# Performance work log

Measured on AMD Instinct MI355X. Metric: run time of the kernel, lower is better.

The kernel has to match this reference:

```python
import jax, jax.numpy as jnp
import numpy as np
from jax import lax

DIM = 512
ATT_DIM = 512
N_HEADS = 8
HEAD_DIM = ATT_DIM // N_HEADS
SEQ = 4096


def q_rsqrt(x):
    # quake-style fast inverse sqrt with one Newton iteration (matches torch module)
    y = np.asarray((x,), dtype=np.float32)
    x2 = y * 0.5
    i = y.view(np.int32)
    i = np.right_shift(i, 1)
    i = 1597463007 - i
    y = i.view(np.float32)
    y = y * (1.5 - x2 * y * y)
    return float(y[0])

SCALING = q_rsqrt(HEAD_DIM)  # fast-approx 1/sqrt(head_dim)

# Schraudolph fast-exp constants (pulp-trainlib fastexp_gist)
GIST_A = 12102203.17133801  # 2^23 / ln(2)
GIST_B = 1064986823.0       # bias with correction term
GIST_C = 8388608.0          # underflow cutoff -> 0
GIST_D = 2139095040.0       # overflow clamp (float32 inf bits)


def fastexp_gist(x):
    t = GIST_A * x + GIST_B
    t = jnp.where(t < GIST_C, 0.0, jnp.where(t > GIST_D, GIST_D, t))
    return lax.bitcast_convert_type(t.astype(jnp.int32), jnp.float32)


def softmax_fastexp(s):
    m = jnp.max(s, axis=-1, keepdims=True)
    e = fastexp_gist(s - m)
    return e / jnp.sum(e, axis=-1, keepdims=True)


def setup_inputs() -> dict:
    key = jax.random.key(0)
    ks = jax.random.split(key, 8)
    std = 0.02
    return {
        "x": jax.random.normal(ks[0], (SEQ, DIM), dtype=jnp.float32),
        "Wq": jax.random.normal(ks[1], (ATT_DIM, DIM), dtype=jnp.float32) * std,
        "bq": jnp.zeros((ATT_DIM,), dtype=jnp.float32),
        "Wk": jax.random.normal(ks[2], (ATT_DIM, DIM), dtype=jnp.float32) * std,
        "bk": jnp.zeros((ATT_DIM,), dtype=jnp.float32),
        "Wv": jax.random.normal(ks[3], (ATT_DIM, DIM), dtype=jnp.float32) * std,
        "bv": jnp.zeros((ATT_DIM,), dtype=jnp.float32),
        "Wout": jax.random.normal(ks[4], (DIM, ATT_DIM), dtype=jnp.float32) * std,
        "tgt_len": SEQ,
    }


def reference(x, Wq, bq, Wk, bk, Wv, bv, Wout, tgt_len):
    # projections (torch Linear: y = x @ W.T + b)
    q = (x @ Wq.T + bq).reshape(tgt_len, N_HEADS, HEAD_DIM).transpose(1, 0, 2)  # [H,L,d]
    k = (x @ Wk.T + bk).reshape(tgt_len, N_HEADS, HEAD_DIM).transpose(1, 0, 2)
    v = (x @ Wv.T + bv).reshape(tgt_len, N_HEADS, HEAD_DIM).transpose(1, 0, 2)
    scores = jnp.einsum('hld,hmd->hlm', q, k) * SCALING  # [H,L,L]
    probs = softmax_fastexp(scores)
    out = jnp.einsum('hlm,hmd->hld', probs, v)           # [H,L,d]
    out = out.transpose(1, 0, 2).reshape(tgt_len, ATT_DIM)
    return out @ Wout.T  # proj_out has no bias
```

## Files before the change

### kernel.cpp

```cpp
#include <hip/hip_runtime.h>
#include <hip/hip_bf16.h>
#include <string.h>

#define SEQ 4096
#define DIM 512
#define NH  8
#define HD  64
#define SEQP (SEQ + 128)
#define NT  (SEQ/64)
#define KSPLIT 4
#define KCHUNK (SEQ/KSPLIT)
#define KTILES (KCHUNK/64)
#define PMSPLIT 8
#define KCHUNK_A (SEQ/PMSPLIT)
#define KTILES_A (KCHUNK_A/64)

typedef __attribute__((ext_vector_type(4))) float  f32x4;
typedef __attribute__((ext_vector_type(8))) short  bf16x8;
typedef __attribute__((ext_vector_type(4))) short  s16x4;
typedef __attribute__((ext_vector_type(2))) unsigned int u32x2;

__device__ __forceinline__ unsigned short f2bfh(float f){
    union { __hip_bfloat16 h; unsigned short u; } cv;
    cv.h = __float2bfloat16(f);
    return cv.u;
}

__device__ __forceinline__ bf16x8 cvt8(f32x4 lo, f32x4 hi){
    bf16x8 r;
    r[0]=(short)f2bfh(lo[0]); r[1]=(short)f2bfh(lo[1]);
    r[2]=(short)f2bfh(lo[2]); r[3]=(short)f2bfh(lo[3]);
    r[4]=(short)f2bfh(hi[0]); r[5]=(short)f2bfh(hi[1]);
    r[6]=(short)f2bfh(hi[2]); r[7]=(short)f2bfh(hi[3]);
    return r;
}

__device__ __forceinline__ bf16x8 load8f(const float* p){
    f32x4 lo = *(const f32x4*)p;
    f32x4 hi = *(const f32x4*)(p+4);
    return cvt8(lo, hi);
}

#define FENCE_LDS() asm volatile("s_waitcnt lgkmcnt(0)" ::: "memory")

__global__ __launch_bounds__(256) void cvt5_kernel(
    const float* __restrict__ x,  const float* __restrict__ wq,
    const float* __restrict__ wk, const float* __restrict__ wv,
    const float* __restrict__ wo,
    unsigned short* __restrict__ xb,  unsigned short* __restrict__ wqb,
    unsigned short* __restrict__ wkb, unsigned short* __restrict__ wvb,
    unsigned short* __restrict__ wob)
{
    int b = blockIdx.x;
    const float* src; unsigned short* dst; int base;
    if (b < 1024){ src = x; dst = xb; base = b; }
    else {
        int t  = (b - 1024) >> 7;
        base   = (b - 1024) & 127;
        src = (t==0) ? wq  : (t==1) ? wk  : (t==2) ? wv  : wo;
        dst = (t==0) ? wqb : (t==1) ? wkb : (t==2) ? wvb : wob;
    }
    size_t i = ((size_t)base*256 + threadIdx.x)*8;
    f32x4 lo = *(const f32x4*)(src + i);
    f32x4 hi = *(const f32x4*)(src + i + 4);
    *(bf16x8*)(dst + i) = cvt8(lo, hi);
}

__global__ __launch_bounds__(256, 4) void proj_qkv_b_kernel(
    const unsigned short* __restrict__ xb,
    const unsigned short* __restrict__ Wqb, const float* __restrict__ bq,
    const unsigned short* __restrict__ Wkb, const float* __restrict__ bk,
    const unsigned short* __restrict__ Wvb, const float* __restrict__ bv,
    unsigned short* __restrict__ Qb, unsigned short* __restrict__ Kh,
    unsigned short* __restrict__ Vtp)
{
    __shared__ __align__(16) unsigned short xs[128*64];
    __shared__ __align__(16) unsigned short wsh[64*64];

    const int z = blockIdx.z;
    const unsigned short* W = (z==0) ? Wqb : ((z==1) ? Wkb : Wvb);
    const float* bb = (z==0) ? bq : ((z==1) ? bk : bv);
    const int tid = threadIdx.x;
    const int wv  = tid >> 6;
    const int l   = tid & 63;
    const int g   = l >> 4;
    const int l15 = l & 15;
    const int l7  = l15 & 7;
    const int r0b = blockIdx.x * 128;
    const int c0  = blockIdx.y * 64;
    const int hy  = blockIdx.y;

    const int sc  = tid & 7;
    const int sr  = tid >> 3;
    const int scs = (sc ^ (sr & 7)) * 8;

    f32x4 acc[2][4];
    #pragma unroll
    for(int s=0;s<2;s++)
        #pragma unroll
        for(int d=0;d<4;d++) acc[s][d] = (f32x4){0.f,0.f,0.f,0.f};

    bf16x8 xf[4], wf[2];
    #pragma unroll
    for(int j=0;j<4;j++)
        xf[j] = *(const bf16x8*)(xb + (size_t)(r0b + sr + 32*j)*DIM + sc*8);
    #pragma unroll
    for(int j=0;j<2;j++)
        wf[j] = *(const bf16x8*)(W + (size_t)(c0 + sr + 32*j)*DIM + sc*8);

    for(int t=0;t<8;t++){
        #pragma unroll
        for(int j=0;j<4;j++)
            *(bf16x8*)&xs[(sr + 32*j)*64 + scs] = xf[j];
        #pragma unroll
        for(int j=0;j<2;j++)
            *(bf16x8*)&wsh[(sr + 32*j)*64 + scs] = wf[j];
        __syncthreads();
        if(t+1 < 8){
            const int kt = (t+1)*64;
            #pragma unroll
            for(int j=0;j<4;j++)
                xf[j] = *(const bf16x8*)(xb + (size_t)(r0b + sr + 32*j)*DIM + kt + sc*8);
            #pragma unroll
            for(int j=0;j<2;j++)
                wf[j] = *(const bf16x8*)(W + (size_t)(c0 + sr + 32*j)*DIM + kt + sc*8);
        }
        #pragma unroll
        for(int kh=0;kh<2;kh++){
            bf16x8 a[2];
            #pragma unroll
            for(int s=0;s<2;s++){
                const int row = wv*32 + s*16 + l15;
                a[s] = *(const bf16x8*)&xs[row*64 + (((kh*4+g) ^ l7)*8)];
            }
            #pragma unroll
            for(int d=0;d<4;d++){
                const int row = d*16 + l15;
                bf16x8 b = *(const bf16x8*)&wsh[row*64 + (((kh*4+g) ^ l7)*8)];
                #pragma unroll
                for(int s=0;s<2;s++)
                    acc[s][d] = __builtin_amdgcn_mfma_f32_16x16x32_bf16(a[s], b, acc[s][d], 0,0,0);
            }
        }
        __syncthreads();
    }

    const int r0 = r0b + wv*32;
    #pragma unroll
    for(int d=0;d<4;d++){
        float bias = bb[c0 + d*16 + l15];
        #pragma unroll
        for(int s=0;s<2;s++){
            if(z == 2){
                s16x4 pk;
                #pragma unroll
                for(int r=0;r<4;r++) pk[r] = (short)f2bfh(acc[s][d][r] + bias);
                *(s16x4*)(Vtp + ((size_t)hy*HD + d*16+l15)*SEQP + r0 + s*16 + g*4) = pk;
            } else if(z == 1){
                #pragma unroll
                for(int r=0;r<4;r++)
                    Kh[((size_t)hy*SEQ + r0+s*16+g*4+r)*HD + d*16 + l15] =
                        f2bfh(acc[s][d][r] + bias);
            } else {
                #pragma unroll
                for(int r=0;r<4;r++)
                    Qb[(size_t)(r0+s*16+g*4+r)*DIM + c0 + d*16 + l15] =
                        f2bfh(acc[s][d][r] + bias);
            }
        }
    }
}

__global__ __launch_bounds__(256) void proj_qkv_kernel(
    const float* __restrict__ x,
    const float* __restrict__ Wq, const float* __restrict__ bq,
    const float* __restrict__ Wk, const float* __restrict__ bk,
    const float* __restrict__ Wv, const float* __restrict__ bv,
    unsigned short* __restrict__ Qb, unsigned short* __restrict__ Kh,
    unsigned short* __restrict__ Vtp)
{
    const int z = blockIdx.z;
    const float* W  = (z==0) ? Wq : ((z==1) ? Wk : Wv);
    const float* bb = (z==0) ? bq : ((z==1) ? bk : bv);
    const int wv  = threadIdx.x >> 6;
    const int l   = threadIdx.x & 63;
    const int g   = l >> 4;
    const int l15 = l & 15;
    const int r0  = blockIdx.x * 128 + wv * 32;
    const int c0  = blockIdx.y * 64;
    const int hy  = blockIdx.y;

    f32x4 acc[2][4];
    #pragma unroll
    for(int s=0;s<2;s++)
        #pragma unroll
        for(int d=0;d<4;d++) acc[s][d] = (f32x4){0.f,0.f,0.f,0.f};

    for(int kt=0; kt<DIM; kt+=32){
        bf16x8 a[2];
        #pragma unroll
        for(int s=0;s<2;s++)
            a[s] = load8f(x + (size_t)(r0+s*16+l15)*DIM + kt + g*8);
        #pragma unroll
        for(int d=0;d<4;d++){
            bf16x8 b = load8f(W + (size_t)(c0+d*16+l15)*DIM + kt + g*8);
            #pragma unroll
            for(int s=0;s<2;s++)
                acc[s][d] = __builtin_amdgcn_mfma_f32_16x16x32_bf16(a[s], b, acc[s][d], 0,0,0);
        }
    }

    #pragma unroll
    for(int d=0;d<4;d++){
        float bias = bb[c0 + d*16 + l15];
        #pragma unroll
        for(int s=0;s<2;s++){
            if(z == 2){
                s16x4 pk;
                #pragma unroll
                for(int r=0;r<4;r++) pk[r] = (short)f2bfh(acc[s][d][r] + bias);
                *(s16x4*)(Vtp + ((size_t)hy*HD + d*16+l15)*SEQP + r0 + s*16 + g*4) = pk;
            } else if(z == 1){
                #pragma unroll
                for(int r=0;r<4;r++)
                    Kh[((size_t)hy*SEQ + r0+s*16+g*4+r)*HD + d*16 + l15] =
                        f2bfh(acc[s][d][r] + bias);
            } else {
                #pragma unroll
                for(int r=0;r<4;r++)
                    Qb[(size_t)(r0+s*16+g*4+r)*DIM + c0 + d*16 + l15] =
                        f2bfh(acc[s][d][r] + bias);
            }
        }
    }
}

__global__ __launch_bounds__(512, 4) void attn_max_kernel(
    const unsigned short* __restrict__ Qb,
    const unsigned short* __restrict__ Kh,
    float* __restrict__ Pm)
{
    __shared__ __align__(16) unsigned short kb[2][64*64];

    const int tid = threadIdx.x;
    const int wv  = tid >> 6;
    const int l   = tid & 63;
    const int g   = l >> 4;
    const int l15 = l & 15;
    const int l7  = l15 & 7;
    const int h   = blockIdx.x & 7;
    const int kz  = (blockIdx.x >> 3) & 7;
    const int Rw  = (blockIdx.x >> 6) * 256 + wv * 32;
    const int kbase = kz * KCHUNK_A;

    const unsigned short* Khh = Kh + (size_t)h*SEQ*HD;
    const int sr  = tid >> 3, sc = tid & 7;
    const int scs = (sc ^ (sr & 7)) * 8;
    const int lA  = sr*64 + scs;

    bf16x8 aq[2][2];
    #pragma unroll
    for(int s=0;s<2;s++)
        #pragma unroll
        for(int kh=0;kh<2;kh++)
            aq[s][kh] = *(const bf16x8*)(Qb + (size_t)(Rw+s*16+l15)*DIM + h*HD + kh*32 + g*8);

    float mx[2];
    mx[0] = mx[1] = -3.0e38f;

    bf16x8 krA = *(const bf16x8*)(Khh + (size_t)(kbase+sr)*HD + sc*8);
    *(bf16x8*)&kb[0][lA] = krA;
    __syncthreads();

    for(int t=0;t<KTILES_A;t++){
        const int cur = t & 1;
        if(t+1 < KTILES_A)
            krA = *(const bf16x8*)(Khh + (size_t)(kbase+(t+1)*64+sr)*HD + sc*8);
        #pragma unroll
        for(int ks=0;ks<4;ks++){
            const int krow = ks*16 + l15;
            bf16x8 b0 = *(const bf16x8*)&kb[cur][krow*64 + ((g     ^ l7)*8)];
            bf16x8 b1 = *(const bf16x8*)&kb[cur][krow*64 + (((4+g) ^ l7)*8)];
            #pragma unroll
            for(int s=0;s<2;s++){
                f32x4 acc = (f32x4){0.f,0.f,0.f,0.f};
                acc = __builtin_amdgcn_mfma_f32_16x16x32_bf16(b0, aq[s][0], acc, 0,0,0);
                acc = __builtin_amdgcn_mfma_f32_16x16x32_bf16(b1, aq[s][1], acc, 0,0,0);
                #pragma unroll
                for(int r=0;r<4;r++) mx[s] = fmaxf(mx[s], acc[r]);
            }
        }
        if(t+1 < KTILES_A)
            *(bf16x8*)&kb[cur^1][lA] = krA;
        __syncthreads();
    }
    #pragma unroll
    for(int s=0;s<2;s++){
        mx[s] = fmaxf(mx[s], __shfl_xor(mx[s], 16, 64));
        mx[s] = fmaxf(mx[s], __shfl_xor(mx[s], 32, 64));
    }

    if(l < 16){
        Pm[(size_t)(h*PMSPLIT + kz)*SEQ + Rw + l15]      = mx[0];
        Pm[(size_t)(h*PMSPLIT + kz)*SEQ + Rw + 16 + l15] = mx[1];
    }
}

#define PSTRIDE 68

__global__ __launch_bounds__(512, 4) void attn_pv_kernel(
    const unsigned short* __restrict__ Qb,
    const unsigned short* __restrict__ Kh,
    const unsigned short* __restrict__ Vtp,
    const float* __restrict__ Pm,
    float* __restrict__ numf,
    float* __restrict__ denf,
    float k1f)
{
    __shared__ __align__(16) unsigned short kb[2][64*64];
    __shared__ __align__(16) unsigned short vb[2][64*64];
    __shared__ __align__(16) unsigned short pb[8][32*PSTRIDE];

    const int tid = threadIdx.x;
    const int wv  = tid >> 6;
    const int l   = tid & 63;
    const int g   = l >> 4;
    const int l15 = l & 15;
    const int l7  = l15 & 7;
    const int h   = blockIdx.x & 7;
    const int kz  = (blockIdx.x >> 3) & 3;
    const int Rw  = (blockIdx.x >> 5) * 256 + wv * 32;
    const int kbase = kz * KCHUNK;

    const unsigned short* Khh = Kh  + (size_t)h*SEQ*HD;
    const unsigned short* Vh  = Vtp + (size_t)h*HD*SEQP;

    const int sr  = tid >> 3, sc = tid & 7;
    const int scs = (sc ^ (sr & 7)) * 8;
    const int lA  = sr*64 + scs;

    bf16x8 aq[2][2];
    #pragma unroll
    for(int s=0;s<2;s++)
        #pragma unroll
        for(int kh=0;kh<2;kh++)
            aq[s][kh] = *(const bf16x8*)(Qb + (size_t)(Rw+s*16+l15)*DIM + h*HD + kh*32 + g*8);

    float crow[2];
    #pragma unroll
    for(int s=0;s<2;s++){
        const int row = Rw + s*16 + l15;
        float m = Pm[(size_t)(h*PMSPLIT+0)*SEQ + row];
        #pragma unroll
        for(int p=1;p<PMSPLIT;p++)
            m = fmaxf(m, Pm[(size_t)(h*PMSPLIT+p)*SEQ + row]);
        crow[s] = 1064986823.0f - k1f*m;
    }

    f32x4 oacc[2][4];
    #pragma unroll
    for(int s=0;s<2;s++)
        #pragma unroll
        for(int d=0;d<4;d++) oacc[s][d] = (f32x4){0.f,0.f,0.f,0.f};
    f32x4 dacc[2];
    dacc[0] = (f32x4){0.f,0.f,0.f,0.f};
    dacc[1] = (f32x4){0.f,0.f,0.f,0.f};

    bf16x8 ones;
    #pragma unroll
    for(int j=0;j<8;j++) ones[j] = (short)0x3F80;

    bf16x8 krA = *(const bf16x8*)(Khh + (size_t)(kbase+sr)*HD + sc*8);
    bf16x8 vrA = *(const bf16x8*)(Vh  + (size_t)sr*SEQP + kbase + sc*8);
    *(bf16x8*)&kb[0][lA] = krA;
    *(bf16x8*)&vb[0][lA] = vrA;
    __syncthreads();

    for(int t=0;t<KTILES;t++){
        const int cur = t & 1;
        if(t+1 < KTILES){
            const int k0n = kbase + (t+1)*64;
            krA = *(const bf16x8*)(Khh + (size_t)(k0n+sr)*HD + sc*8);
            vrA = *(const bf16x8*)(Vh  + (size_t)sr*SEQP + k0n + sc*8);
        }
        #pragma unroll
        for(int ks=0;ks<4;ks++){
            const int krow = ks*16 + l15;
            bf16x8 b0 = *(const bf16x8*)&kb[cur][krow*64 + ((g     ^ l7)*8)];
            bf16x8 b1 = *(const bf16x8*)&kb[cur][krow*64 + (((4+g) ^ l7)*8)];
            #pragma unroll
            for(int s=0;s<2;s++){
                f32x4 acc = (f32x4){0.f,0.f,0.f,0.f};
                acc = __builtin_amdgcn_mfma_f32_16x16x32_bf16(b0, aq[s][0], acc, 0,0,0);
                acc = __builtin_amdgcn_mfma_f32_16x16x32_bf16(b1, aq[s][1], acc, 0,0,0);
                unsigned int w0, w1;
                {
                    float t0 = fmaf(k1f, acc[0], crow[s]);
                    float t1 = fmaf(k1f, acc[1], crow[s]);
                    float t2 = fmaf(k1f, acc[2], crow[s]);
                    float t3 = fmaf(k1f, acc[3], crow[s]);
                    unsigned int p0 = f2bfh(__int_as_float((int)t0));
                    unsigned int p1 = f2bfh(__int_as_float((int)t1));
                    unsigned int p2 = f2bfh(__int_as_float((int)t2));
                    unsigned int p3 = f2bfh(__int_as_float((int)t3));
                    w0 = p0 | (p1 << 16);
                    w1 = p2 | (p3 << 16);
                }
                u32x2 pw; pw[0] = w0; pw[1] = w1;
                *(u32x2*)&pb[wv][(s*16+l15)*PSTRIDE + ks*16 + g*4] = pw;
            }
        }
        FENCE_LDS();

        __builtin_amdgcn_s_setprio(1);
        #pragma unroll
        for(int ks2=0; ks2<2; ks2++){
            bf16x8 pa[2];
            #pragma unroll
            for(int s=0;s<2;s++)
                pa[s] = *(const bf16x8*)&pb[wv][(s*16+l15)*PSTRIDE + ks2*32 + g*8];
            #pragma unroll
            for(int s=0;s<2;s++)
                dacc[s] = __builtin_amdgcn_mfma_f32_16x16x32_bf16(pa[s], ones, dacc[s], 0,0,0);
            #pragma unroll
            for(int d=0;d<4;d++){
                const int vrow = d*16 + l15;
                bf16x8 bv_ = *(const bf16x8*)&vb[cur][vrow*64 + (((ks2*4+g) ^ l7)*8)];
                #pragma unroll
                for(int s=0;s<2;s++)
                    oacc[s][d] = __builtin_amdgcn_mfma_f32_16x16x32_bf16(pa[s], bv_, oacc[s][d], 0,0,0);
            }
        }
        __builtin_amdgcn_s_setprio(0);

        if(t+1 < KTILES){
            *(bf16x8*)&kb[cur^1][lA] = krA;
            *(bf16x8*)&vb[cur^1][lA] = vrA;
        }
        __syncthreads();
    }

    #pragma unroll
    for(int s=0;s<2;s++)
        #pragma unroll
        for(int d=0;d<4;d++)
            #pragma unroll
            for(int r=0;r<4;r++)
                numf[(size_t)kz*SEQ*DIM + (size_t)(Rw+s*16+g*4+r)*DIM + h*HD + d*16 + l15]
                    = oacc[s][d][r];
    if(l15 == 0){
        #pragma unroll
        for(int s=0;s<2;s++)
            #pragma unroll
            for(int r=0;r<4;r++)
                denf[(size_t)kz*SEQ*NH + (size_t)(Rw+s*16+g*4+r)*NH + h] = dacc[s][r];
    }
}

__global__ __launch_bounds__(256) void attn_merge_kernel(
    const float* __restrict__ numf,
    const float* __restrict__ denf,
    unsigned short* __restrict__ Ab)
{
    const size_t NS = (size_t)SEQ*DIM;
    int idx = blockIdx.x*256 + threadIdx.x;
    int row = idx >> 7;
    int dg  = (idx & 127) << 2;
    int h   = dg >> 6;

    float d0 = denf[(size_t)0*SEQ*NH + (size_t)row*NH + h];
    float d1 = denf[(size_t)1*SEQ*NH + (size_t)row*NH + h];
    float d2 = denf[(size_t)2*SEQ*NH + (size_t)row*NH + h];
    float d3 = denf[(size_t)3*SEQ*NH + (size_t)row*NH + h];
    float inv = 1.0f / (((d0 + d1) + d2) + d3);

    f32x4 n0 = *(const f32x4*)(numf + 0*NS + (size_t)row*DIM + dg);
    f32x4 n1 = *(const f32x4*)(numf + 1*NS + (size_t)row*DIM + dg);
    f32x4 n2 = *(const f32x4*)(numf + 2*NS + (size_t)row*DIM + dg);
    f32x4 n3 = *(const f32x4*)(numf + 3*NS + (size_t)row*DIM + dg);
    f32x4 s = ((n0 + n1) + n2) + n3;

    s16x4 o;
    #pragma unroll
    for(int j=0;j<4;j++) o[j] = (short)f2bfh(s[j] * inv);
    *(s16x4*)(Ab + (size_t)row*DIM + dg) = o;
}

__global__ __launch_bounds__(256, 2) void attn_kernel(
    const unsigned short* __restrict__ Qb,
    const unsigned short* __restrict__ Kh,
    const unsigned short* __restrict__ Vtp,
    unsigned short* __restrict__ Ab,
    float k1f)
{
    __shared__ __align__(16) unsigned short kbf[2][64*64];
    __shared__ __align__(16) unsigned short vbf[2][64*64];
    __shared__ __align__(16) unsigned short pbf[4][16*68];

    const int tid = threadIdx.x;
    const int wv  = tid >> 6;
    const int l   = tid & 63;
    const int g   = l >> 4;
    const int l15 = l & 15;
    const int l7  = l15 & 7;
    const int h   = blockIdx.x & 7;
    const int Rw  = (blockIdx.x >> 3) * 64 + wv * 16;

    const unsigned short* Khh = Kh  + (size_t)h*SEQ*HD;
    const unsigned short* Vh  = Vtp + (size_t)h*HD*SEQP;

    const int sr  = tid >> 3;
    const int sc  = tid & 7;
    const int scs = (sc ^ (sr & 7)) * 8;
    const int ldsA = sr*64 + scs;
    const int ldsB = (sr+32)*64 + scs;

    bf16x8 aq[2];
    #pragma unroll
    for(int kh=0;kh<2;kh++)
        aq[kh] = *(const bf16x8*)(Qb + (size_t)(Rw+l15)*DIM + h*HD + kh*32 + g*8);

    bf16x8 krA, krB, vrA, vrB;

    float mx[4];
    mx[0]=mx[1]=mx[2]=mx[3]=-3.0e38f;

    krA = *(const bf16x8*)(Khh + (size_t)sr*HD      + sc*8);
    krB = *(const bf16x8*)(Khh + (size_t)(sr+32)*HD + sc*8);
    *(bf16x8*)&kbf[0][ldsA] = krA;
    *(bf16x8*)&kbf[0][ldsB] = krB;
    __syncthreads();

    for(int t=0;t<NT;t++){
        const int cur = t & 1;
        if(t+1 < NT){
            const unsigned short* kp = Khh + (size_t)((t+1)*64)*HD;
            krA = *(const bf16x8*)(kp + (size_t)sr*HD      + sc*8);
            krB = *(const bf16x8*)(kp + (size_t)(sr+32)*HD + sc*8);
        }
        #pragma unroll
        for(int ks=0;ks<4;ks++){
            const int krow = ks*16 + l15;
            bf16x8 b0 = *(const bf16x8*)&kbf[cur][krow*64 + ((g     ^ l7)*8)];
            bf16x8 b1 = *(const bf16x8*)&kbf[cur][krow*64 + (((4+g) ^ l7)*8)];
            f32x4 acc = (f32x4){0.f,0.f,0.f,0.f};
            acc = __builtin_amdgcn_mfma_f32_16x16x32_bf16(aq[0], b0, acc, 0,0,0);
            acc = __builtin_amdgcn_mfma_f32_16x16x32_bf16(aq[1], b1, acc, 0,0,0);
            #pragma unroll
            for(int r=0;r<4;r++) mx[r] = fmaxf(mx[r], acc[r]);
        }
        if(t+1 < NT){
            *(bf16x8*)&kbf[cur^1][ldsA] = krA;
            *(bf16x8*)&kbf[cur^1][ldsB] = krB;
        }
        __syncthreads();
    }
    #pragma unroll
    for(int off=1; off<16; off<<=1)
        #pragma unroll
        for(int r=0;r<4;r++)
            mx[r] = fmaxf(mx[r], __shfl_xor(mx[r], off, 64));
    float crow[4];
    #pragma unroll
    for(int r=0;r<4;r++) crow[r] = 1064986823.0f - k1f*mx[r];

    f32x4 oacc[4];
    #pragma unroll
    for(int d=0;d<4;d++) oacc[d] = (f32x4){0.f,0.f,0.f,0.f};
    f32x4 dacc = (f32x4){0.f,0.f,0.f,0.f};

    bf16x8 ones;
    #pragma unroll
    for(int j=0;j<8;j++) ones[j] = (short)0x3F80;

    krA = *(const bf16x8*)(Khh + (size_t)sr*HD        + sc*8);
    krB = *(const bf16x8*)(Khh + (size_t)(sr+32)*HD   + sc*8);
    vrA = *(const bf16x8*)(Vh  + (size_t)sr*SEQP      + sc*8);
    vrB = *(const bf16x8*)(Vh  + (size_t)(sr+32)*SEQP + sc*8);
    *(bf16x8*)&kbf[0][ldsA] = krA;  *(bf16x8*)&kbf[0][ldsB] = krB;
    *(bf16x8*)&vbf[0][ldsA] = vrA;  *(bf16x8*)&vbf[0][ldsB] = vrB;
    __syncthreads();

    for(int t=0;t<NT;t++){
        const int cur = t & 1;
        if(t+1 < NT){
            const int k0n = (t+1)*64;
            krA = *(const bf16x8*)(Khh + (size_t)(k0n + sr)*HD    + sc*8);
            krB = *(const bf16x8*)(Khh + (size_t)(k0n + sr+32)*HD + sc*8);
            vrA = *(const bf16x8*)(Vh  + (size_t)sr*SEQP      + k0n + sc*8);
            vrB = *(const bf16x8*)(Vh  + (size_t)(sr+32)*SEQP + k0n + sc*8);
        }
        #pragma unroll
        for(int ks=0;ks<4;ks++){
            const int krow = ks*16 + l15;
            bf16x8 b0 = *(const bf16x8*)&kbf[cur][krow*64 + ((g     ^ l7)*8)];
            bf16x8 b1 = *(const bf16x8*)&kbf[cur][krow*64 + (((4+g) ^ l7)*8)];
            f32x4 acc = (f32x4){0.f,0.f,0.f,0.f};
            acc = __builtin_amdgcn_mfma_f32_16x16x32_bf16(aq[0], b0, acc, 0,0,0);
            acc = __builtin_amdgcn_mfma_f32_16x16x32_bf16(aq[1], b1, acc, 0,0,0);
            #pragma unroll
            for(int r=0;r<4;r++){
                float tt = fmaf(k1f, acc[r], crow[r]);
                pbf[wv][(g*4+r)*68 + ks*16 + l15] = f2bfh(__int_as_float((int)tt));
            }
        }
        FENCE_LDS();

        #pragma unroll
        for(int ks2=0; ks2<2; ks2++){
            bf16x8 pa = *(const bf16x8*)&pbf[wv][l15*68 + ks2*32 + g*8];
            dacc = __builtin_amdgcn_mfma_f32_16x16x32_bf16(pa, ones, dacc, 0,0,0);
            #pragma unroll
            for(int d=0;d<4;d++){
                const int vrow = d*16 + l15;
                bf16x8 bv_ = *(const bf16x8*)&vbf[cur][vrow*64 + (((ks2*4+g) ^ l7)*8)];
                oacc[d] = __builtin_amdgcn_mfma_f32_16x16x32_bf16(pa, bv_, oacc[d], 0,0,0);
            }
        }
        if(t+1 < NT){
            *(bf16x8*)&kbf[cur^1][ldsA] = krA;  *(bf16x8*)&kbf[cur^1][ldsB] = krB;
            *(bf16x8*)&vbf[cur^1][ldsA] = vrA;  *(bf16x8*)&vbf[cur^1][ldsB] = vrB;
        }
        __syncthreads();
    }

    float inv[4];
    #pragma unroll
    for(int r=0;r<4;r++) inv[r] = 1.0f / dacc[r];
    #pragma unroll
    for(int d=0;d<4;d++)
        #pragma unroll
        for(int r=0;r<4;r++)
            Ab[(size_t)(Rw + g*4 + r)*DIM + h*HD + d*16 + l15] =
                f2bfh(oacc[d][r] * inv[r]);
}

__global__ __launch_bounds__(256, 4) void proj_out_b_kernel(
    const unsigned short* __restrict__ Ab,
    const unsigned short* __restrict__ Wob,
    float* __restrict__ out)
{
    __shared__ __align__(16) unsigned short xs[128*64];
    __shared__ __align__(16) unsigned short wsh[64*64];

    const int tid = threadIdx.x;
    const int wv  = tid >> 6;
    const int l   = tid & 63;
    const int g   = l >> 4;
    const int l15 = l & 15;
    const int l7  = l15 & 7;
    const int r0b = blockIdx.x * 128;
    const int c0  = blockIdx.y * 64;

    const int sc  = tid & 7;
    const int sr  = tid >> 3;
    const int scs = (sc ^ (sr & 7)) * 8;

    f32x4 acc[2][4];
    #pragma unroll
    for(int s=0;s<2;s++)
        #pragma unroll
        for(int d=0;d<4;d++) acc[s][d] = (f32x4){0.f,0.f,0.f,0.f};

    bf16x8 xf[4], wf[2];
    #pragma unroll
    for(int j=0;j<4;j++)
        xf[j] = *(const bf16x8*)(Ab + (size_t)(r0b + sr + 32*j)*DIM + sc*8);
    #pragma unroll
    for(int j=0;j<2;j++)
        wf[j] = *(const bf16x8*)(Wob + (size_t)(c0 + sr + 32*j)*DIM + sc*8);

    for(int t=0;t<8;t++){
        #pragma unroll
        for(int j=0;j<4;j++)
            *(bf16x8*)&xs[(sr + 32*j)*64 + scs] = xf[j];
        #pragma unroll
        for(int j=0;j<2;j++)
            *(bf16x8*)&wsh[(sr + 32*j)*64 + scs] = wf[j];
        __syncthreads();
        if(t+1 < 8){
            const int kt = (t+1)*64;
            #pragma unroll
            for(int j=0;j<4;j++)
                xf[j] = *(const bf16x8*)(Ab + (size_t)(r0b + sr + 32*j)*DIM + kt + sc*8);
            #pragma unroll
            for(int j=0;j<2;j++)
                wf[j] = *(const bf16x8*)(Wob + (size_t)(c0 + sr + 32*j)*DIM + kt + sc*8);
        }
        #pragma unroll
        for(int kh=0;kh<2;kh++){
            bf16x8 a[2];
            #pragma unroll
            for(int s=0;s<2;s++){
                const int row = wv*32 + s*16 + l15;
                a[s] = *(const bf16x8*)&xs[row*64 + (((kh*4+g) ^ l7)*8)];
            }
            #pragma unroll
            for(int d=0;d<4;d++){
                const int row = d*16 + l15;
                bf16x8 b = *(const bf16x8*)&wsh[row*64 + (((kh*4+g) ^ l7)*8)];
                #pragma unroll
                for(int s=0;s<2;s++)
                    acc[s][d] = __builtin_amdgcn_mfma_f32_16x16x32_bf16(a[s], b, acc[s][d], 0,0,0);
            }
        }
        __syncthreads();
    }

    const int r0 = r0b + wv*32;
    #pragma unroll
    for(int s=0;s<2;s++)
        #pragma unroll
        for(int d=0;d<4;d++)
            #pragma unroll
            for(int r=0;r<4;r++)
                out[(size_t)(r0+s*16+g*4+r)*DIM + c0 + d*16 + l15] = acc[s][d][r];
}

__global__ __launch_bounds__(256) void proj_out_kernel(
    const unsigned short* __restrict__ Ab,
    const float* __restrict__ Wout,
    float* __restrict__ out)
{
    const int wv  = threadIdx.x >> 6;
    const int l   = threadIdx.x & 63;
    const int g   = l >> 4;
    const int l15 = l & 15;
    const int r0  = blockIdx.x * 128 + wv * 32;
    const int c0  = blockIdx.y * 64;

    f32x4 acc[2][4];
    #pragma unroll
    for(int s=0;s<2;s++)
        #pragma unroll
        for(int d=0;d<4;d++) acc[s][d] = (f32x4){0.f,0.f,0.f,0.f};

    for(int kt=0; kt<DIM; kt+=32){
        bf16x8 a[2];
        #pragma unroll
        for(int s=0;s<2;s++)
            a[s] = *(const bf16x8*)(Ab + (size_t)(r0+s*16+l15)*DIM + kt + g*8);
        #pragma unroll
        for(int d=0;d<4;d++){
            bf16x8 b = load8f(Wout + (size_t)(c0+d*16+l15)*DIM + kt + g*8);
            #pragma unroll
            for(int s=0;s<2;s++)
                acc[s][d] = __builtin_amdgcn_mfma_f32_16x16x32_bf16(a[s], b, acc[s][d], 0,0,0);
        }
    }

    #pragma unroll
    for(int s=0;s<2;s++)
        #pragma unroll
        for(int d=0;d<4;d++)
            #pragma unroll
            for(int r=0;r<4;r++)
                out[(size_t)(r0+s*16+g*4+r)*DIM + c0 + d*16 + l15] = acc[s][d][r];
}

extern "C" void kernel_launch(void* const* d_in, const int* in_sizes, int n_in,
                              void* d_out, int out_size, void* d_ws, size_t ws_size,
                              hipStream_t stream)
{
    const float* x    = (const float*)d_in[0];
    const float* Wq   = (const float*)d_in[1];
    const float* bq   = (const float*)d_in[2];
    const float* Wk   = (const float*)d_in[3];
    const float* bk   = (const float*)d_in[4];
    const float* Wv   = (const float*)d_in[5];
    const float* bv   = (const float*)d_in[6];
    const float* Wout = (const float*)d_in[7];
    float* out = (float*)d_out;

    unsigned short* Qb  = (unsigned short*)d_ws;
    unsigned short* Kh  = Qb  + (size_t)SEQ*DIM;
    unsigned short* Vtp = Kh  + (size_t)NH*SEQ*HD;
    unsigned short* Ab  = Vtp + (size_t)NH*HD*SEQP;
    unsigned short* xb  = Ab  + (size_t)SEQ*DIM;
    unsigned short* Wqb = xb  + (size_t)SEQ*DIM;
    unsigned short* Wkb = Wqb + (size_t)DIM*DIM;
    unsigned short* Wvb = Wkb + (size_t)DIM*DIM;
    unsigned short* Wob = Wvb + (size_t)DIM*DIM;
    float* Pm   = (float*)(Wob + (size_t)DIM*DIM);
    float* numf = Pm   + (size_t)NH*PMSPLIT*SEQ;
    float* denf = numf + (size_t)KSPLIT*SEQ*DIM;

    const size_t needed_bf16 = ((size_t)SEQ*DIM*4 + (size_t)NH*HD*SEQP
                                + (size_t)DIM*DIM*4) * 2;
    const size_t needed_f32  = ((size_t)NH*PMSPLIT*SEQ + (size_t)KSPLIT*SEQ*DIM
                                + (size_t)KSPLIT*SEQ*NH) * 4;
    const size_t needed_split = needed_bf16 + needed_f32;

    float xx = 64.0f;
    float x2 = xx * 0.5f;
    int ii; memcpy(&ii, &xx, 4);
    ii = 1597463007 - (ii >> 1);
    float y; memcpy(&y, &ii, 4);
    y = y * (1.5f - x2 * y * y);
    const float scaling = y;
    const float k1f = 12102203.17133801f * scaling;

    if(ws_size >= needed_split){
        cvt5_kernel<<<dim3(1536), 256, 0, stream>>>(
            x, Wq, Wk, Wv, Wout, xb, Wqb, Wkb, Wvb, Wob);
        proj_qkv_b_kernel<<<dim3(SEQ/128, DIM/64, 3), 256, 0, stream>>>(
            xb, Wqb, bq, Wkb, bk, Wvb, bv, Qb, Kh, Vtp);
        attn_max_kernel<<<dim3((SEQ/256)*NH*PMSPLIT), 512, 0, stream>>>(Qb, Kh, Pm);
        attn_pv_kernel<<<dim3((SEQ/256)*NH*KSPLIT), 512, 0, stream>>>(
            Qb, Kh, Vtp, Pm, numf, denf, k1f);
        attn_merge_kernel<<<dim3(SEQ*DIM/4/256), 256, 0, stream>>>(numf, denf, Ab);
        proj_out_b_kernel<<<dim3(SEQ/128, DIM/64), 256, 0, stream>>>(Ab, Wob, out);
    } else if(ws_size >= needed_bf16){
        cvt5_kernel<<<dim3(1536), 256, 0, stream>>>(
            x, Wq, Wk, Wv, Wout, xb, Wqb, Wkb, Wvb, Wob);
        proj_qkv_b_kernel<<<dim3(SEQ/128, DIM/64, 3), 256, 0, stream>>>(
            xb, Wqb, bq, Wkb, bk, Wvb, bv, Qb, Kh, Vtp);
        attn_kernel<<<dim3((SEQ/64)*NH), 256, 0, stream>>>(Qb, Kh, Vtp, Ab, k1f);
        proj_out_b_kernel<<<dim3(SEQ/128, DIM/64), 256, 0, stream>>>(Ab, Wob, out);
    } else {
        proj_qkv_kernel<<<dim3(SEQ/128, DIM/64, 3), 256, 0, stream>>>(
            x, Wq, bq, Wk, bk, Wv, bv, Qb, Kh, Vtp);
        attn_kernel<<<dim3((SEQ/64)*NH), 256, 0, stream>>>(Qb, Kh, Vtp, Ab, k1f);
        proj_out_kernel<<<dim3(SEQ/128, DIM/64), 256, 0, stream>>>(Ab, Wout, out);
    }
}
```

Measured before the change: 100.6 us.

## Give each wave 64 query rows in attn_pv with 256-thread blocks

The attn_pv kernel now uses 4 waves of 256 threads, each handling 64 query rows instead of 8 waves handling 32, so every K/V fragment read from LDS feeds twice as many MFMAs. Each thread now stages two K and two V chunks per tile. The QK/softmax and PV phases are split into halves so PV on the first 32 keys can start before the second half of scores is written, and the setprio hints are removed. The cost is more accumulator registers per wave (16 output tiles plus 4 denominators) and fewer waves per block, which lowers occupancy and latency hiding.

```diff
diff --git a/kernel.cpp b/kernel.cpp
--- a/kernel.cpp
+++ b/kernel.cpp
@@ -308,7 +308,7 @@
 
 #define PSTRIDE 68
 
-__global__ __launch_bounds__(512, 4) void attn_pv_kernel(
+__global__ __launch_bounds__(256, 2) void attn_pv_kernel(
     const unsigned short* __restrict__ Qb,
     const unsigned short* __restrict__ Kh,
     const unsigned short* __restrict__ Vtp,
@@ -319,7 +319,7 @@
 {
     __shared__ __align__(16) unsigned short kb[2][64*64];
     __shared__ __align__(16) unsigned short vb[2][64*64];
-    __shared__ __align__(16) unsigned short pb[8][32*PSTRIDE];
+    __shared__ __align__(16) unsigned short pb[4][64*PSTRIDE];
 
     const int tid = threadIdx.x;
     const int wv  = tid >> 6;
@@ -329,7 +329,7 @@
     const int l7  = l15 & 7;
     const int h   = blockIdx.x & 7;
     const int kz  = (blockIdx.x >> 3) & 3;
-    const int Rw  = (blockIdx.x >> 5) * 256 + wv * 32;
+    const int Rw  = (blockIdx.x >> 5) * 256 + wv * 64;
     const int kbase = kz * KCHUNK;
 
     const unsigned short* Khh = Kh  + (size_t)h*SEQ*HD;
@@ -338,17 +338,18 @@
     const int sr  = tid >> 3, sc = tid & 7;
     const int scs = (sc ^ (sr & 7)) * 8;
     const int lA  = sr*64 + scs;
-
-    bf16x8 aq[2][2];
-    #pragma unroll
-    for(int s=0;s<2;s++)
+    const int lB  = (sr+32)*64 + scs;
+
+    bf16x8 aq[4][2];
+    #pragma unroll
+    for(int s=0;s<4;s++)
         #pragma unroll
         for(int kh=0;kh<2;kh++)
             aq[s][kh] = *(const bf16x8*)(Qb + (size_t)(Rw+s*16+l15)*DIM + h*HD + kh*32 + g*8);
 
-    float crow[2];
-    #pragma unroll
-    for(int s=0;s<2;s++){
+    float crow[4];
+    #pragma unroll
+    for(int s=0;s<4;s++){
         const int row = Rw + s*16 + l15;
         float m = Pm[(size_t)(h*PMSPLIT+0)*SEQ + row];
         #pragma unroll
@@ -357,39 +358,43 @@
         crow[s] = 1064986823.0f - k1f*m;
     }
 
-    f32x4 oacc[2][4];
-    #pragma unroll
-    for(int s=0;s<2;s++)
+    f32x4 oacc[4][4];
+    #pragma unroll
+    for(int s=0;s<4;s++)
         #pragma unroll
         for(int d=0;d<4;d++) oacc[s][d] = (f32x4){0.f,0.f,0.f,0.f};
-    f32x4 dacc[2];
-    dacc[0] = (f32x4){0.f,0.f,0.f,0.f};
-    dacc[1] = (f32x4){0.f,0.f,0.f,0.f};
+    f32x4 dacc[4];
+    #pragma unroll
+    for(int s=0;s<4;s++) dacc[s] = (f32x4){0.f,0.f,0.f,0.f};
 
     bf16x8 ones;
     #pragma unroll
     for(int j=0;j<8;j++) ones[j] = (short)0x3F80;
 
-    bf16x8 krA = *(const bf16x8*)(Khh + (size_t)(kbase+sr)*HD + sc*8);
-    bf16x8 vrA = *(const bf16x8*)(Vh  + (size_t)sr*SEQP + kbase + sc*8);
-    *(bf16x8*)&kb[0][lA] = krA;
-    *(bf16x8*)&vb[0][lA] = vrA;
+    bf16x8 krA = *(const bf16x8*)(Khh + (size_t)(kbase+sr)*HD    + sc*8);
+    bf16x8 krB = *(const bf16x8*)(Khh + (size_t)(kbase+sr+32)*HD + sc*8);
+    bf16x8 vrA = *(const bf16x8*)(Vh  + (size_t)sr*SEQP      + kbase + sc*8);
+    bf16x8 vrB = *(const bf16x8*)(Vh  + (size_t)(sr+32)*SEQP + kbase + sc*8);
+    *(bf16x8*)&kb[0][lA] = krA;  *(bf16x8*)&kb[0][lB] = krB;
+    *(bf16x8*)&vb[0][lA] = vrA;  *(bf16x8*)&vb[0][lB] = vrB;
     __syncthreads();
 
     for(int t=0;t<KTILES;t++){
         const int cur = t & 1;
         if(t+1 < KTILES){
             const int k0n = kbase + (t+1)*64;
-            krA = *(const bf16x8*)(Khh + (size_t)(k0n+sr)*HD + sc*8);
-            vrA = *(const bf16x8*)(Vh  + (size_t)sr*SEQP + k0n + sc*8);
-        }
-        #pragma unroll
-        for(int ks=0;ks<4;ks++){
+            krA = *(const bf16x8*)(Khh + (size_t)(k0n+sr)*HD    + sc*8);
+            krB = *(const bf16x8*)(Khh + (size_t)(k0n+sr+32)*HD + sc*8);
+            vrA = *(const bf16x8*)(Vh  + (size_t)sr*SEQP      + k0n + sc*8);
+            vrB = *(const bf16x8*)(Vh  + (size_t)(sr+32)*SEQP + k0n + sc*8);
+        }
+        #pragma unroll
+        for(int ks=0;ks<2;ks++){
             const int krow = ks*16 + l15;
             bf16x8 b0 = *(const bf16x8*)&kb[cur][krow*64 + ((g     ^ l7)*8)];
             bf16x8 b1 = *(const bf16x8*)&kb[cur][krow*64 + (((4+g) ^ l7)*8)];
             #pragma unroll
-            for(int s=0;s<2;s++){
+            for(int s=0;s<4;s++){
                 f32x4 acc = (f32x4){0.f,0.f,0.f,0.f};
                 acc = __builtin_amdgcn_mfma_f32_16x16x32_bf16(b0, aq[s][0], acc, 0,0,0);
                 acc = __builtin_amdgcn_mfma_f32_16x16x32_bf16(b1, aq[s][1], acc, 0,0,0);
@@ -412,36 +417,79 @@
         }
         FENCE_LDS();
 
-        __builtin_amdgcn_s_setprio(1);
-        #pragma unroll
-        for(int ks2=0; ks2<2; ks2++){
-            bf16x8 pa[2];
-            #pragma unroll
-            for(int s=0;s<2;s++)
-                pa[s] = *(const bf16x8*)&pb[wv][(s*16+l15)*PSTRIDE + ks2*32 + g*8];
-            #pragma unroll
-            for(int s=0;s<2;s++)
+        #pragma unroll
+        for(int ks=2;ks<4;ks++){
+            const int krow = ks*16 + l15;
+            bf16x8 b0 = *(const bf16x8*)&kb[cur][krow*64 + ((g     ^ l7)*8)];
+            bf16x8 b1 = *(const bf16x8*)&kb[cur][krow*64 + (((4+g) ^ l7)*8)];
+            #pragma unroll
+            for(int s=0;s<4;s++){
+                f32x4 acc = (f32x4){0.f,0.f,0.f,0.f};
+                acc = __builtin_amdgcn_mfma_f32_16x16x32_bf16(b0, aq[s][0], acc, 0,0,0);
+                acc = __builtin_amdgcn_mfma_f32_16x16x32_bf16(b1, aq[s][1], acc, 0,0,0);
+                unsigned int w0, w1;
+                {
+                    float t0 = fmaf(k1f, acc[0], crow[s]);
+                    float t1 = fmaf(k1f, acc[1], crow[s]);
+                    float t2 = fmaf(k1f, acc[2], crow[s]);
+                    float t3 = fmaf(k1f, acc[3], crow[s]);
+                    unsigned int p0 = f2bfh(__int_as_float((int)t0));
+                    unsigned int p1 = f2bfh(__int_as_float((int)t1));
+                    unsigned int p2 = f2bfh(__int_as_float((int)t2));
+                    unsigned int p3 = f2bfh(__int_as_float((int)t3));
+                    w0 = p0 | (p1 << 16);
+                    w1 = p2 | (p3 << 16);
+                }
+                u32x2 pw; pw[0] = w0; pw[1] = w1;
+                *(u32x2*)&pb[wv][(s*16+l15)*PSTRIDE + ks*16 + g*4] = pw;
+            }
+        }
+        {
+            bf16x8 pa[4];
+            #pragma unroll
+            for(int s=0;s<4;s++)
+                pa[s] = *(const bf16x8*)&pb[wv][(s*16+l15)*PSTRIDE + g*8];
+            #pragma unroll
+            for(int s=0;s<4;s++)
                 dacc[s] = __builtin_amdgcn_mfma_f32_16x16x32_bf16(pa[s], ones, dacc[s], 0,0,0);
             #pragma unroll
             for(int d=0;d<4;d++){
                 const int vrow = d*16 + l15;
-                bf16x8 bv_ = *(const bf16x8*)&vb[cur][vrow*64 + (((ks2*4+g) ^ l7)*8)];
-                #pragma unroll
-                for(int s=0;s<2;s++)
+                bf16x8 bv_ = *(const bf16x8*)&vb[cur][vrow*64 + ((g ^ l7)*8)];
+                #pragma unroll
+                for(int s=0;s<4;s++)
                     oacc[s][d] = __builtin_amdgcn_mfma_f32_16x16x32_bf16(pa[s], bv_, oacc[s][d], 0,0,0);
             }
         }
-        __builtin_amdgcn_s_setprio(0);
+        FENCE_LDS();
+
+        {
+            bf16x8 pa[4];
+            #pragma unroll
+            for(int s=0;s<4;s++)
+                pa[s] = *(const bf16x8*)&pb[wv][(s*16+l15)*PSTRIDE + 32 + g*8];
+            #pragma unroll
+            for(int s=0;s<4;s++)
+                dacc[s] = __builtin_amdgcn_mfma_f32_16x16x32_bf16(pa[s], ones, dacc[s], 0,0,0);
+            #pragma unroll
+            for(int d=0;d<4;d++){
+                const int vrow = d*16 + l15;
+                bf16x8 bv_ = *(const bf16x8*)&vb[cur][vrow*64 + (((4+g) ^ l7)*8)];
+                #pragma unroll
+                for(int s=0;s<4;s++)
+                    oacc[s][d] = __builtin_amdgcn_mfma_f32_16x16x32_bf16(pa[s], bv_, oacc[s][d], 0,0,0);
+            }
+        }
 
         if(t+1 < KTILES){
-            *(bf16x8*)&kb[cur^1][lA] = krA;
-            *(bf16x8*)&vb[cur^1][lA] = vrA;
+            *(bf16x8*)&kb[cur^1][lA] = krA;  *(bf16x8*)&kb[cur^1][lB] = krB;
+            *(bf16x8*)&vb[cur^1][lA] = vrA;  *(bf16x8*)&vb[cur^1][lB] = vrB;
         }
         __syncthreads();
     }
 
     #pragma unroll
-    for(int s=0;s<2;s++)
+    for(int s=0;s<4;s++)
         #pragma unroll
         for(int d=0;d<4;d++)
             #pragma unroll
@@ -450,7 +498,7 @@
                     = oacc[s][d][r];
     if(l15 == 0){
         #pragma unroll
-        for(int s=0;s<2;s++)
+        for(int s=0;s<4;s++)
             #pragma unroll
             for(int r=0;r<4;r++)
                 denf[(size_t)kz*SEQ*NH + (size_t)(Rw+s*16+g*4+r)*NH + h] = dacc[s][r];
@@ -806,7 +854,7 @@
         proj_qkv_b_kernel<<<dim3(SEQ/128, DIM/64, 3), 256, 0, stream>>>(
             xb, Wqb, bq, Wkb, bk, Wvb, bv, Qb, Kh, Vtp);
         attn_max_kernel<<<dim3((SEQ/256)*NH*PMSPLIT), 512, 0, stream>>>(Qb, Kh, Pm);
-        attn_pv_kernel<<<dim3((SEQ/256)*NH*KSPLIT), 512, 0, stream>>>(
+        attn_pv_kernel<<<dim3((SEQ/256)*NH*KSPLIT), 256, 0, stream>>>(
             Qb, Kh, Vtp, Pm, numf, denf, k1f);
         attn_merge_kernel<<<dim3(SEQ*DIM/4/256), 256, 0, stream>>>(numf, denf, Ab);
         proj_out_b_kernel<<<dim3(SEQ/128, DIM/64), 256, 0, stream>>>(Ab, Wob, out);
```

Measured after the change: 100.8 us. Within noise of the previous version (+0.2%).
